# Performance work log

Measured on AMD Instinct MI355X. Metric: run time of the kernel, lower is better.

The kernel has to match this reference:

```python
import jax, jax.numpy as jnp
import numpy as np

D_MODEL = 1024
NUM_HEADS = 16
HEAD_DIM = D_MODEL // NUM_HEADS


def setup_inputs() -> dict:
    key = jax.random.key(0)
    ks = jax.random.split(key, 5)
    s = 1.0 / np.sqrt(D_MODEL)
    return {
        "x": jax.random.normal(ks[0], (4, 2048, D_MODEL), dtype=jnp.float32),
        "w_qkv": jax.random.uniform(ks[1], (3 * D_MODEL, D_MODEL), jnp.float32, -s, s),
        "b_qkv": jax.random.uniform(ks[2], (3 * D_MODEL,), jnp.float32, -s, s),
        "w_out": jax.random.uniform(ks[3], (D_MODEL, D_MODEL), jnp.float32, -s, s),
        "b_out": jax.random.uniform(ks[4], (D_MODEL,), jnp.float32, -s, s),
    }


def reference(x, w_qkv, b_qkv, w_out, b_out):
    B, T, D = x.shape
    # torch Linear: y = x @ W^T + b
    qkv = x @ w_qkv.T + b_qkv                                  # [B,T,3D]
    qkv = qkv.reshape(B, T, 3, NUM_HEADS, HEAD_DIM)
    q, k, v = jnp.moveaxis(qkv, 2, 0)                          # each [B,T,H,Hd]
    q = q.transpose(0, 2, 1, 3)                                # [B,H,T,Hd]
    k = k.transpose(0, 2, 1, 3)
    v = v.transpose(0, 2, 1, 3)
    scale = 1.0 / np.sqrt(HEAD_DIM).astype(np.float32)
    scores = jnp.einsum("bhqd,bhkd->bhqk", q, k) * scale       # [B,H,T,T]
    attn = jax.nn.softmax(scores, axis=-1)
    out = jnp.einsum("bhqk,bhkd->bhqd", attn, v)               # [B,H,T,Hd]
    out = out.transpose(0, 2, 1, 3).reshape(B, T, D)
    return out @ w_out.T + b_out
```

## Files before the change

### kernel.cpp

```cpp
#include <hip/hip_runtime.h>
#include <hip/hip_bf16.h>

#define SEQLEN  2048
#define DMODEL  1024
#define NHEADS  16
#define BT_ROWS 8192

typedef __attribute__((ext_vector_type(8))) _Float16 half8;
typedef __attribute__((ext_vector_type(4))) _Float16 half4;
typedef __attribute__((ext_vector_type(4))) float f32x4;
typedef unsigned short u16;

#define MFMAH(A, B, C)  __builtin_amdgcn_mfma_f32_16x16x32_f16((A), (B), (C), 0, 0, 0)

static __device__ __forceinline__ float fast_exp2(float x) {
#if __has_builtin(__builtin_amdgcn_exp2f)
    return __builtin_amdgcn_exp2f(x);
#else
    return exp2f(x);
#endif
}

typedef const __attribute__((address_space(1))) unsigned int* gas_t;
typedef __attribute__((address_space(3))) unsigned int* las_t;
static __device__ __forceinline__ void gld16(const void* g, void* l) {
    __builtin_amdgcn_global_load_lds((gas_t)g, (las_t)l, 16, 0, 0);
}

__global__ __launch_bounds__(256)
void cvt_f16(const float* __restrict__ in, u16* __restrict__ outp, int n4)
{
    int i = blockIdx.x * 256 + threadIdx.x;
    const int stride = gridDim.x * 256;
    for (; i < n4; i += stride) {
        const float4 v = ((const float4*)in)[i];
        const float f[4] = {v.x, v.y, v.z, v.w};
        ushort4 h4;
        u16 hh[4];
#pragma unroll
        for (int j = 0; j < 4; ++j)
            hh[j] = __builtin_bit_cast(u16, (_Float16)f[j]);
        h4.x = hh[0]; h4.y = hh[1]; h4.z = hh[2]; h4.w = hh[3];
        *(ushort4*)(outp + (size_t)i * 4) = h4;
    }
}

template<int MODE>
__global__ __launch_bounds__(256)
void gemm_nt_mfma(const u16* __restrict__ Af, const u16* __restrict__ Bf,
                  const float* __restrict__ bias, float* __restrict__ Cf,
                  u16* __restrict__ Pq, u16* __restrict__ Pk,
                  u16* __restrict__ Pv)
{
    __shared__ _Float16 Ah[128 * 32];
    __shared__ _Float16 Bh[128 * 32];

    const int tid  = threadIdx.x;
    const int lane = tid & 63;
    const int w    = tid >> 6;
    const int l15  = lane & 15;
    const int lg   = lane >> 4;
    const int wm   = w & 1;
    const int wn   = w >> 1;
    const int rowBase = blockIdx.y * 128;
    const int colBase = blockIdx.x * 128;

    const int srow = lane >> 2;
    const int sc   = lane & 3;

    f32x4 acc[4][4];
#pragma unroll
    for (int m = 0; m < 4; ++m)
#pragma unroll
        for (int n = 0; n < 4; ++n) acc[m][n] = (f32x4){0.f, 0.f, 0.f, 0.f};

    auto stage = [&](int kt) {
        const int k0 = kt * 32;
#pragma unroll
        for (int i = 0; i < 2; ++i) {
            const int slab = w * 2 + i;
            const int row  = slab * 16 + srow;
            const int gc   = sc ^ ((row >> 1) & 3);
            const size_t aoff = (size_t)(rowBase + row) * 1024 + k0 + gc * 8;
            const size_t boff = (size_t)(colBase + row) * 1024 + k0 + gc * 8;
            gld16(Af + aoff, &Ah[slab * 512]);
            gld16(Bf + boff, &Bh[slab * 512]);
        }
    };

    stage(0);

    for (int kt = 0; kt < 32; ++kt) {
        __syncthreads();

        half8 afh[4], bfh[4];
#pragma unroll
        for (int m = 0; m < 4; ++m) {
            const int row = wm * 64 + m * 16 + l15;
            const int cR  = lg ^ ((row >> 1) & 3);
            afh[m] = *(const half8*)&Ah[row * 32 + cR * 8];
        }
#pragma unroll
        for (int n = 0; n < 4; ++n) {
            const int row = wn * 64 + n * 16 + l15;
            const int cR  = lg ^ ((row >> 1) & 3);
            bfh[n] = *(const half8*)&Bh[row * 32 + cR * 8];
        }

        __syncthreads();
        if (kt < 31) stage(kt + 1);

        __builtin_amdgcn_s_setprio(1);
#pragma unroll
        for (int m = 0; m < 4; ++m)
#pragma unroll
            for (int n = 0; n < 4; ++n)
                acc[m][n] = MFMAH(afh[m], bfh[n], acc[m][n]);
        __builtin_amdgcn_s_setprio(0);
    }

    float bv[4];
#pragma unroll
    for (int n = 0; n < 4; ++n)
        bv[n] = bias[colBase + wn * 64 + n * 16 + l15];

    if constexpr (MODE == 0) {
#pragma unroll
        for (int m = 0; m < 4; ++m)
#pragma unroll
            for (int n = 0; n < 4; ++n) {
                const int col = colBase + wn * 64 + n * 16 + l15;
#pragma unroll
                for (int r = 0; r < 4; ++r) {
                    const int row = rowBase + wm * 64 + m * 16 + lg * 4 + r;
                    Cf[(size_t)row * 1024 + col] = acc[m][n][r] + bv[n];
                }
            }
    } else {
        const int comp = colBase >> 10;
        const float scale = (comp == 0) ? (0.125f * 1.44269504f) : 1.0f;
        u16* hp = (comp == 0) ? Pq : ((comp == 1) ? Pk : Pv);
        const int colc0 = colBase & 1023;
#pragma unroll
        for (int m = 0; m < 4; ++m)
#pragma unroll
            for (int n = 0; n < 4; ++n) {
                const int col = colc0 + wn * 64 + n * 16 + l15;
#pragma unroll
                for (int r = 0; r < 4; ++r) {
                    const int row = rowBase + wm * 64 + m * 16 + lg * 4 + r;
                    const float v = (acc[m][n][r] + bv[n]) * scale;
                    hp[(size_t)row * 1024 + col] =
                        __builtin_bit_cast(u16, (_Float16)v);
                }
            }
    }
}

__global__ __launch_bounds__(256, 4)
void flash_attn_mfma(const u16* __restrict__ Qf, const u16* __restrict__ Kf,
                     const u16* __restrict__ Vf, u16* __restrict__ Of)
{
    __shared__ __align__(16) _Float16 Kh[64 * 64];
    __shared__ __align__(16) _Float16 Vt[64][72];
    __shared__ __align__(16) _Float16 Pl[4][32][72];

    const int tid  = threadIdx.x;
    const int lane = tid & 63;
    const int w    = tid >> 6;
    const int l15  = lane & 15;
    const int lg   = lane >> 4;

    const int raw = blockIdx.x;
    const int swz = (raw & 7) * 128 + (raw >> 3);
    const int bh  = swz >> 4;
    const int qb  = swz & 15;
    const int b   = bh >> 4;
    const int h   = bh & 15;

    const int qRow0 = b * SEQLEN + qb * 128;
    const int kRowB = b * SEQLEN;
    const int hc    = h * 64;

    half8 Qr[2][2];
#pragma unroll
    for (int qt = 0; qt < 2; ++qt)
#pragma unroll
        for (int g = 0; g < 2; ++g) {
            const size_t off = (size_t)(qRow0 + w * 32 + qt * 16 + l15) * 1024
                             + hc + g * 32 + lg * 8;
            Qr[qt][g] = *(const half8*)(Qf + off);
        }

    f32x4 O[2][4];
    float lsum[2][4];
#pragma unroll
    for (int qt = 0; qt < 2; ++qt)
#pragma unroll
        for (int r = 0; r < 4; ++r) lsum[qt][r] = 0.0f;
#pragma unroll
    for (int qt = 0; qt < 2; ++qt)
#pragma unroll
        for (int dt = 0; dt < 4; ++dt) O[qt][dt] = (f32x4){0.f, 0.f, 0.f, 0.f};

    const int kvc = lane;
    const int vcp = (kvc & 15) * 4 + (kvc >> 4);
    const int dr0 = w * 16;

    half8 kreg[2], vreg0, vreg1;
    int krow[2], kcc[2];

    auto load_tile = [&](int kt) {
#pragma unroll
        for (int i = 0; i < 2; ++i) {
            const int s = tid + 256 * i;
            const int row = s >> 3;
            const int c   = s & 7;
            krow[i] = row; kcc[i] = c;
            const int gc = c ^ (row & 7);
            const size_t g = (size_t)(kRowB + kt * 64 + row) * 1024 + hc + gc * 8;
            kreg[i] = *(const half8*)(Kf + g);
        }
        const size_t g = (size_t)(kRowB + kt * 64 + kvc) * 1024 + hc + dr0;
        vreg0 = *(const half8*)(Vf + g);
        vreg1 = *(const half8*)(Vf + g + 8);
    };

    load_tile(0);

    for (int kt = 0; kt < SEQLEN / 64; ++kt) {
        __syncthreads();
#pragma unroll
        for (int i = 0; i < 2; ++i)
            *(half8*)&Kh[krow[i] * 64 + kcc[i] * 8] = kreg[i];
#pragma unroll
        for (int j = 0; j < 8; ++j) Vt[dr0 + j][vcp] = vreg0[j];
#pragma unroll
        for (int j = 0; j < 8; ++j) Vt[dr0 + 8 + j][vcp] = vreg1[j];
        __syncthreads();

        if (kt < SEQLEN / 64 - 1) load_tile(kt + 1);

        f32x4 S[2][4];
#pragma unroll
        for (int qt = 0; qt < 2; ++qt)
#pragma unroll
            for (int k4 = 0; k4 < 4; ++k4) S[qt][k4] = (f32x4){0.f, 0.f, 0.f, 0.f};

        __builtin_amdgcn_s_setprio(1);
#pragma unroll
        for (int k4 = 0; k4 < 4; ++k4) {
            const int row = k4 * 16 + l15;
            const int swk = row & 7;
            const half8 kf0 = *(const half8*)&Kh[row * 64 + ((lg     ^ swk) * 8)];
            const half8 kf1 = *(const half8*)&Kh[row * 64 + (((4+lg) ^ swk) * 8)];
#pragma unroll
            for (int qt = 0; qt < 2; ++qt) {
                f32x4 a = S[qt][k4];
                a = MFMAH(Qr[qt][0], kf0, a);
                a = MFMAH(Qr[qt][1], kf1, a);
                S[qt][k4] = a;
            }
        }
        __builtin_amdgcn_s_setprio(0);

#pragma unroll
        for (int qt = 0; qt < 2; ++qt) {
#pragma unroll
            for (int r = 0; r < 4; ++r) {
                const float p0 = fast_exp2(S[qt][0][r]);
                const float p1 = fast_exp2(S[qt][1][r]);
                const float p2 = fast_exp2(S[qt][2][r]);
                const float p3 = fast_exp2(S[qt][3][r]);
                lsum[qt][r] += (p0 + p1) + (p2 + p3);
                half4 pk;
                pk[0] = (_Float16)p0; pk[1] = (_Float16)p1;
                pk[2] = (_Float16)p2; pk[3] = (_Float16)p3;
                *(half4*)&Pl[w][qt * 16 + lg * 4 + r][l15 * 4] = pk;
            }
        }

        asm volatile("s_waitcnt lgkmcnt(0)" ::: "memory");
        __builtin_amdgcn_sched_barrier(0);

        __builtin_amdgcn_s_setprio(1);
#pragma unroll
        for (int ks = 0; ks < 2; ++ks) {
            half8 Pf[2];
#pragma unroll
            for (int qt = 0; qt < 2; ++qt)
                Pf[qt] = *(const half8*)&Pl[w][qt * 16 + l15][ks * 32 + lg * 8];
#pragma unroll
            for (int dt = 0; dt < 4; ++dt) {
                const half8 Vfr = *(const half8*)&Vt[dt * 16 + l15][ks * 32 + lg * 8];
#pragma unroll
                for (int qt = 0; qt < 2; ++qt)
                    O[qt][dt] = MFMAH(Pf[qt], Vfr, O[qt][dt]);
            }
        }
        __builtin_amdgcn_s_setprio(0);
    }

#pragma unroll
    for (int qt = 0; qt < 2; ++qt)
#pragma unroll
        for (int r = 0; r < 4; ++r) {
            float rs = lsum[qt][r];
            rs += __shfl_xor(rs, 1);
            rs += __shfl_xor(rs, 2);
            rs += __shfl_xor(rs, 4);
            rs += __shfl_xor(rs, 8);
            lsum[qt][r] = rs;
        }

#pragma unroll
    for (int qt = 0; qt < 2; ++qt)
#pragma unroll
        for (int r = 0; r < 4; ++r) {
            const float inv = 1.0f / lsum[qt][r];
            const int row = qRow0 + w * 32 + qt * 16 + lg * 4 + r;
#pragma unroll
            for (int dt = 0; dt < 4; ++dt) {
                const float o = O[qt][dt][r] * inv;
                const size_t off = (size_t)row * 1024 + hc + dt * 16 + l15;
                Of[off] = __builtin_bit_cast(u16, (_Float16)o);
            }
        }
}

extern "C" void kernel_launch(void* const* d_in, const int* in_sizes, int n_in,
                              void* d_out, int out_size, void* d_ws, size_t ws_size,
                              hipStream_t stream)
{
    const float* x     = (const float*)d_in[0];
    const float* w_qkv = (const float*)d_in[1];
    const float* b_qkv = (const float*)d_in[2];
    const float* w_out = (const float*)d_in[3];
    const float* b_out = (const float*)d_in[4];
    float* out = (float*)d_out;

    const size_t PLANE = (size_t)BT_ROWS * DMODEL;
    u16* Qf  = (u16*)d_ws;
    u16* Kf  = Qf + PLANE;
    u16* Vf  = Kf + PLANE;
    u16* xF  = Vf + PLANE;
    u16* aF  = xF;
    u16* wqkvF = xF + PLANE;
    u16* woutF = wqkvF + (size_t)3072 * 1024;

    cvt_f16<<<2048, 256, 0, stream>>>(x, xF, (int)(PLANE / 4));
    cvt_f16<<<768, 256, 0, stream>>>(w_qkv, wqkvF, 3072 * 1024 / 4);
    cvt_f16<<<256, 256, 0, stream>>>(w_out, woutF, 1024 * 1024 / 4);

    gemm_nt_mfma<1><<<dim3(3072 / 128, BT_ROWS / 128), 256, 0, stream>>>(
        xF, wqkvF, b_qkv, nullptr, Qf, Kf, Vf);

    flash_attn_mfma<<<dim3(1024), 256, 0, stream>>>(Qf, Kf, Vf, aF);

    gemm_nt_mfma<0><<<dim3(DMODEL / 128, BT_ROWS / 128), 256, 0, stream>>>(
        aF, woutF, b_out, out, nullptr, nullptr, nullptr);
}
```

Before: 210.6 us.

## Compute softmax row sums via MFMA with ones, pack V and P stores

Result: faster. 205.6 us (-2.4%).

```diff
diff --git a/kernel.cpp b/kernel.cpp
--- a/kernel.cpp
+++ b/kernel.cpp
@@ -8,6 +8,7 @@
 
 typedef __attribute__((ext_vector_type(8))) _Float16 half8;
 typedef __attribute__((ext_vector_type(4))) _Float16 half4;
+typedef __attribute__((ext_vector_type(2))) _Float16 half2v;
 typedef __attribute__((ext_vector_type(4))) float f32x4;
 typedef unsigned short u16;
 
@@ -25,6 +26,10 @@
 typedef __attribute__((address_space(3))) unsigned int* las_t;
 static __device__ __forceinline__ void gld16(const void* g, void* l) {
     __builtin_amdgcn_global_load_lds((gas_t)g, (las_t)l, 16, 0, 0);
+}
+
+static __device__ __forceinline__ unsigned pack_f16x2(float a, float b) {
+    return __builtin_bit_cast(unsigned, __builtin_amdgcn_cvt_pkrtz(a, b));
 }
 
 __global__ __launch_bounds__(256)
@@ -193,19 +198,21 @@
         }
 
     f32x4 O[2][4];
-    float lsum[2][4];
-#pragma unroll
-    for (int qt = 0; qt < 2; ++qt)
-#pragma unroll
-        for (int r = 0; r < 4; ++r) lsum[qt][r] = 0.0f;
-#pragma unroll
-    for (int qt = 0; qt < 2; ++qt)
+    f32x4 accL[2];
+#pragma unroll
+    for (int qt = 0; qt < 2; ++qt) {
+        accL[qt] = (f32x4){0.f, 0.f, 0.f, 0.f};
 #pragma unroll
         for (int dt = 0; dt < 4; ++dt) O[qt][dt] = (f32x4){0.f, 0.f, 0.f, 0.f};
-
-    const int kvc = lane;
-    const int vcp = (kvc & 15) * 4 + (kvc >> 4);
-    const int dr0 = w * 16;
+    }
+    half8 vones;
+#pragma unroll
+    for (int j = 0; j < 8; ++j) vones[j] = (_Float16)1.0f;
+
+    const int vp  = tid & 31;
+    const int kv0 = (vp & 15) | ((vp >> 4) << 5);
+    const int pcol = (kv0 & 15) * 4 + (kv0 >> 4);
+    const int d0  = (tid >> 5) * 8;
 
     half8 kreg[2], vreg0, vreg1;
     int krow[2], kcc[2];
@@ -221,9 +228,9 @@
             const size_t g = (size_t)(kRowB + kt * 64 + row) * 1024 + hc + gc * 8;
             kreg[i] = *(const half8*)(Kf + g);
         }
-        const size_t g = (size_t)(kRowB + kt * 64 + kvc) * 1024 + hc + dr0;
+        const size_t g = (size_t)(kRowB + kt * 64 + kv0) * 1024 + hc + d0;
         vreg0 = *(const half8*)(Vf + g);
-        vreg1 = *(const half8*)(Vf + g + 8);
+        vreg1 = *(const half8*)(Vf + g + (size_t)16 * 1024);
     };
 
     load_tile(0);
@@ -234,9 +241,11 @@
         for (int i = 0; i < 2; ++i)
             *(half8*)&Kh[krow[i] * 64 + kcc[i] * 8] = kreg[i];
 #pragma unroll
-        for (int j = 0; j < 8; ++j) Vt[dr0 + j][vcp] = vreg0[j];
-#pragma unroll
-        for (int j = 0; j < 8; ++j) Vt[dr0 + 8 + j][vcp] = vreg1[j];
+        for (int j = 0; j < 8; ++j) {
+            half2v pv;
+            pv[0] = vreg0[j]; pv[1] = vreg1[j];
+            *(half2v*)&Vt[d0 + j][pcol] = pv;
+        }
         __syncthreads();
 
         if (kt < SEQLEN / 64 - 1) load_tile(kt + 1);
@@ -272,11 +281,10 @@
                 const float p1 = fast_exp2(S[qt][1][r]);
                 const float p2 = fast_exp2(S[qt][2][r]);
                 const float p3 = fast_exp2(S[qt][3][r]);
-                lsum[qt][r] += (p0 + p1) + (p2 + p3);
-                half4 pk;
-                pk[0] = (_Float16)p0; pk[1] = (_Float16)p1;
-                pk[2] = (_Float16)p2; pk[3] = (_Float16)p3;
-                *(half4*)&Pl[w][qt * 16 + lg * 4 + r][l15 * 4] = pk;
+                uint2 pw;
+                pw.x = pack_f16x2(p0, p1);
+                pw.y = pack_f16x2(p2, p3);
+                *(uint2*)&Pl[w][qt * 16 + lg * 4 + r][l15 * 4] = pw;
             }
         }
 
@@ -297,6 +305,9 @@
                 for (int qt = 0; qt < 2; ++qt)
                     O[qt][dt] = MFMAH(Pf[qt], Vfr, O[qt][dt]);
             }
+#pragma unroll
+            for (int qt = 0; qt < 2; ++qt)
+                accL[qt] = MFMAH(Pf[qt], vones, accL[qt]);
         }
         __builtin_amdgcn_s_setprio(0);
     }
@@ -305,19 +316,7 @@
     for (int qt = 0; qt < 2; ++qt)
 #pragma unroll
         for (int r = 0; r < 4; ++r) {
-            float rs = lsum[qt][r];
-            rs += __shfl_xor(rs, 1);
-            rs += __shfl_xor(rs, 2);
-            rs += __shfl_xor(rs, 4);
-            rs += __shfl_xor(rs, 8);
-            lsum[qt][r] = rs;
-        }
-
-#pragma unroll
-    for (int qt = 0; qt < 2; ++qt)
-#pragma unroll
-        for (int r = 0; r < 4; ++r) {
-            const float inv = 1.0f / lsum[qt][r];
+            const float inv = 1.0f / accL[qt][r];
             const int row = qRow0 + w * 32 + qt * 16 + lg * 4 + r;
 #pragma unroll
             for (int dt = 0; dt < 4; ++dt) {
```
